# Performance work log

Hardware: AMD Instinct MI355X
Metric: run time of the kernel (lower is better)

The kernel has to match this reference:

```python
import jax, jax.numpy as jnp
import numpy as np

G, N, E, F, D = 4096, 64, 256, 64, 128
H1, H2 = 16, 2
EP = 32768
EPS = 1e-15
MAX_LOGSTD = 10.0


def setup_inputs() -> dict:
    key = jax.random.key(0)
    ks = jax.random.split(key, 16)
    def lin(k, i, o):
        return (jax.random.normal(k, (i, o), jnp.float32) / np.sqrt(i)).astype(jnp.float32)
    inp = {}
    inp["x"] = jax.random.normal(ks[0], (G, N, F), jnp.float32)
    inp["edge_index"] = jax.random.randint(ks[1], (G, 2, E), 0, N, dtype=jnp.int32)
    inp["edge_weight"] = jax.random.uniform(ks[2], (G, E), jnp.float32)
    inp["pos_edges"] = jax.random.randint(ks[3], (2, EP), 0, G, dtype=jnp.int32)
    inp["neg_edges"] = jax.random.randint(ks[4], (2, EP), 0, G, dtype=jnp.int32)
    inp["eps"] = jax.random.normal(ks[5], (G, D), jnp.float32)
    inp["W_gcn1"] = lin(ks[6], F, D); inp["b_gcn1"] = jnp.zeros((D,), jnp.float32)
    inp["W_fc1"] = lin(ks[7], D, H1); inp["b_fc1"] = jnp.zeros((H1,), jnp.float32)
    inp["W_fc2"] = lin(ks[8], H1, H2); inp["b_fc2"] = jnp.zeros((H2,), jnp.float32)
    inp["W_c1"] = lin(ks[9], D, 2 * D); inp["b_c1"] = jnp.zeros((2 * D,), jnp.float32)
    inp["W_mu"] = lin(ks[10], 2 * D, D); inp["b_mu"] = jnp.zeros((D,), jnp.float32)
    inp["W_ls"] = lin(ks[11], 2 * D, D); inp["b_ls"] = jnp.zeros((D,), jnp.float32)
    inp["emb"] = jax.random.normal(ks[12], (G, D), jnp.float32)
    inp["W_lin1"] = lin(ks[13], 2 * D, 2 * D); inp["b_lin1"] = jnp.zeros((2 * D,), jnp.float32)
    inp["W_lin2"] = lin(ks[14], 2 * D, 2 * D); inp["b_lin2"] = jnp.zeros((2 * D,), jnp.float32)
    return inp


def gcn_conv(x, src, dst, w, W, b, n):
    # PyG GCNConv: add self-loops (weight 1), sym-normalize, aggregate at target (col).
    xw = x @ W                                      # [n, out]
    deg = jnp.zeros((n,), xw.dtype).at[dst].add(w) + 1.0
    dinv = jax.lax.rsqrt(deg)
    norm = dinv[src] * w * dinv[dst]
    agg = jnp.zeros_like(xw).at[dst].add(xw[src] * norm[:, None])
    agg = agg + xw * (dinv * dinv)[:, None]         # self-loop term
    return agg + b


def sage_graph(x, ei, w, W_gcn1, b_gcn1, W_fc1, b_fc1, W_fc2, b_fc2):
    src, dst = ei[0], ei[1]
    h = gcn_conv(x, src, dst, w, W_gcn1, b_gcn1, N)          # [N, D]
    a1 = jnp.tanh(h @ W_fc1 + b_fc1)                         # [N, H1]
    S = jax.nn.softmax(a1 @ W_fc2 + b_fc2, axis=1)           # [N, 2]
    # get_laplacian(normalization='sym'): L = I - D^{-1/2} A D^{-1/2}, deg from row
    deg = jnp.zeros((N,), x.dtype).at[src].add(w)
    dinv = jnp.where(deg > 0, jax.lax.rsqrt(jnp.maximum(deg, 1e-30)), 0.0)
    lw = -dinv[src] * w * dinv[dst]
    L = jnp.zeros((N, N), x.dtype).at[src, dst].add(lw) + jnp.eye(N, dtype=x.dtype)
    new_adj = S.T @ (L @ S)                                  # [2, 2]
    norm_adj = new_adj / jnp.maximum(jnp.sum(jnp.abs(new_adj), axis=1, keepdims=True), 1e-12)
    diag = jnp.diagonal(norm_adj)
    pos_penalty = jnp.mean((diag - 1.0) ** 2)                # MSE vs ones(2)
    g_emb = jnp.mean(S.T @ h, axis=0)                        # [D]
    return g_emb, pos_penalty


def gcn_conv_unw(x, src, dst, W, b, n):
    return gcn_conv(x, src, dst, jnp.ones(src.shape, x.dtype), W, b, n)


def reference(x, edge_index, edge_weight, pos_edges, neg_edges, eps,
              W_gcn1, b_gcn1, W_fc1, b_fc1, W_fc2, b_fc2,
              W_c1, b_c1, W_mu, b_mu, W_ls, b_ls, emb,
              W_lin1, b_lin1, W_lin2, b_lin2):
    g_embs, pens = jax.vmap(sage_graph,
                            in_axes=(0, 0, 0, None, None, None, None, None, None))(
        x, edge_index, edge_weight, W_gcn1, b_gcn1, W_fc1, b_fc1, W_fc2, b_fc2)
    positive_penalty = jnp.mean(pens)
    # VGAE encode over graph-level graph (dropout in eval mode = identity)
    ps, pd = pos_edges[0], pos_edges[1]
    h = jax.nn.relu(gcn_conv_unw(g_embs, ps, pd, W_c1, b_c1, G))
    mu = gcn_conv_unw(h, ps, pd, W_mu, b_mu, G)
    logstd = jnp.minimum(gcn_conv_unw(h, ps, pd, W_ls, b_ls, G), MAX_LOGSTD)
    z = mu + eps * jnp.exp(logstd)                            # reparametrize
    zc = jnp.concatenate([emb, z], axis=-1)                   # [G, 2D]
    def pred(ei):
        fx = zc[ei[0]] @ W_lin1 + b_lin1
        fy = zc[ei[1]] @ W_lin2 + b_lin2
        return jax.nn.sigmoid(jnp.sum(fx * fy, axis=1))
    pos_pred = pred(pos_edges)
    neg_pred = pred(neg_edges)
    rec_loss = -jnp.mean(jnp.log(pos_pred + EPS)) - jnp.mean(jnp.log(1.0 - neg_pred + EPS))
    kl = -0.5 * jnp.mean(jnp.sum(1.0 + 2.0 * logstd - mu ** 2 - jnp.exp(2.0 * logstd), axis=1))
    pre_loss = rec_loss + kl / G
    return pre_loss, positive_penalty, pos_pred, neg_pred
```

## Files before the change

kernel.cpp:

```cpp
#include <hip/hip_runtime.h>
#include <hip/hip_bf16.h>
#include <math.h>

#define GG   4096
#define NNODE 64
#define EEDGE 256
#define FFEAT 64
#define DDIM 128
#define EP   32768

__device__ __forceinline__ float fast_tanh(float x) {
    float e = __expf(2.0f * x);
    return 1.0f - 2.0f / (e + 1.0f);
}

__global__ void k_prep(const float* __restrict__ Wg, const float* __restrict__ Wf1,
                       const float* __restrict__ bf1, const float* __restrict__ bg,
                       float* __restrict__ Wgf1, float* __restrict__ bcomb,
                       float* __restrict__ bg32, int* __restrict__ icnt_g) {
    int t = threadIdx.x;
    for (int o = t; o < 1024; o += 256) {
        int f = o >> 4, j = o & 15;
        float s = 0.f;
        for (int d = 0; d < 128; ++d) s += Wg[f * 128 + d] * Wf1[d * 16 + j];
        Wgf1[o] = s;
    }
    if (t < 16) {
        float s = bf1[t];
        for (int d = 0; d < 128; ++d) s += bg[d] * Wf1[d * 16 + t];
        bcomb[t] = s;
    }
    if (t >= 128) bg32[t - 128] = 32.0f * bg[t - 128];
    for (int i = t; i < 4096; i += 256) icnt_g[i] = 0;
}

__global__ __launch_bounds__(256) void k_y(
    const float* __restrict__ x, const float* __restrict__ W,
    float* __restrict__ Y)
{
    __shared__ __align__(16) float Ws[1024];
    const int t = threadIdx.x;
    *(float4*)&Ws[t * 4] = *(const float4*)&W[t * 4];
    const int rr = t >> 2, q = t & 3;
    const size_t r0 = (size_t)blockIdx.x * 256 + rr;
    const float* x0 = &x[r0 * 64];
    __syncthreads();
    float4 p0 = {0,0,0,0}, p1 = {0,0,0,0}, p2 = {0,0,0,0}, p3 = {0,0,0,0};
#pragma unroll 4
    for (int kb = 0; kb < 16; ++kb) {
        float4 xv0 = *(const float4*)&x0[kb * 4];
        float4 xv1 = *(const float4*)&x0[4096 + kb * 4];
        float4 xv2 = *(const float4*)&x0[8192 + kb * 4];
        float4 xv3 = *(const float4*)&x0[12288 + kb * 4];
#pragma unroll
        for (int kk = 0; kk < 4; ++kk) {
            float4 wv = *(const float4*)&Ws[(kb * 4 + kk) * 16 + q * 4];
            float a0 = (&xv0.x)[kk], a1 = (&xv1.x)[kk];
            float a2 = (&xv2.x)[kk], a3 = (&xv3.x)[kk];
            p0.x += a0 * wv.x; p0.y += a0 * wv.y; p0.z += a0 * wv.z; p0.w += a0 * wv.w;
            p1.x += a1 * wv.x; p1.y += a1 * wv.y; p1.z += a1 * wv.z; p1.w += a1 * wv.w;
            p2.x += a2 * wv.x; p2.y += a2 * wv.y; p2.z += a2 * wv.z; p2.w += a2 * wv.w;
            p3.x += a3 * wv.x; p3.y += a3 * wv.y; p3.z += a3 * wv.z; p3.w += a3 * wv.w;
        }
    }
    float* y0 = &Y[r0 * 16 + q * 4];
    *(float4*)&y0[0]          = p0;
    *(float4*)&y0[64 * 16]    = p1;
    *(float4*)&y0[128 * 16]   = p2;
    *(float4*)&y0[192 * 16]   = p3;
}

__global__ __launch_bounds__(256) void k_pg(
    const float* __restrict__ Yg, const int* __restrict__ ei, const float* __restrict__ ew,
    const float* __restrict__ x, const float* __restrict__ bcomb,
    const float* __restrict__ Wf2, const float* __restrict__ bf2,
    float* __restrict__ Qh, float* __restrict__ pens)
{
    __shared__ __align__(16) float sm[2624];
    float* Ys    = sm;
    int*   lsrc  = (int*)(sm + 1280);
    float* lnrm  = sm + 1536;
    int*   icnt  = (int*)(sm + 1792);
    int*   offs  = (int*)(sm + 1856);
    int*   curs  = (int*)(sm + 1920);
    float* degw  = sm + 1984;
    float* dinvs = sm + 2048;
    float* deg2s = sm + 2112;
    float* dinv2s= sm + 2176;
    float* cws   = sm + 2240;
    float* Ss    = sm + 2304;
    float* LSs   = sm + 2432;
    float* bcs   = sm + 2560;
    float* Wf2s  = sm + 2576;
    float* bf2s  = sm + 2608;

    const int g = blockIdx.x;
    const int t = threadIdx.x;
    const int n = t >> 2, q = t & 3;

    int es, ed; float wv;
    {
        const int* eg = ei + (size_t)g * 512;
        es = eg[t];
        ed = eg[256 + t];
        wv = ew[(size_t)g * 256 + t];
        *(float4*)&Ys[n * 20 + q * 4] = *(const float4*)&Yg[(size_t)g * 1024 + t * 4];
        if (t < 16) bcs[t] = bcomb[t];
        if (t < 32) Wf2s[t] = Wf2[t];
        if (t < 2)  bf2s[t] = bf2[t];
        if (t < 64) { icnt[t] = 0; degw[t] = 1.0f; deg2s[t] = 0.0f; }
        if (t < 128) LSs[t] = 0.0f;
    }
    __syncthreads();

    atomicAdd(&icnt[ed], 1);
    atomicAdd(&degw[ed], wv);
    atomicAdd(&deg2s[es], wv);
    __syncthreads();

    if (t < 64) {
        int v = icnt[t], own = v;
        for (int o = 1; o < 64; o <<= 1) { int u = __shfl_up(v, o); if (t >= o) v += u; }
        int excl = v - own;
        offs[t] = excl; curs[t] = excl;
        float dv = rsqrtf(degw[t]);
        dinvs[t] = dv;
        cws[t] = dv * dv;
        float dg = deg2s[t];
        dinv2s[t] = dg > 0.0f ? rsqrtf(fmaxf(dg, 1e-30f)) : 0.0f;
    }
    __syncthreads();

    float lw;
    {
        int pos = atomicAdd(&curs[ed], 1);
        float nm = dinvs[es] * wv * dinvs[ed];
        lsrc[pos] = es;
        lnrm[pos] = nm;
        atomicAdd(&cws[es], nm);
        lw = -dinv2s[es] * wv * dinv2s[ed];
    }
    __syncthreads();

    {
        float dv = dinvs[n];
        float sc = dv * dv;
        float4 acc = *(const float4*)&Ys[n * 20 + q * 4];
        acc.x *= sc; acc.y *= sc; acc.z *= sc; acc.w *= sc;
        int o = offs[n], c = icnt[n];
        for (int j = 0; j < c; ++j) {
            int s = lsrc[o + j];
            float nm = lnrm[o + j];
            float4 yv = *(const float4*)&Ys[s * 20 + q * 4];
            acc.x += yv.x * nm; acc.y += yv.y * nm;
            acc.z += yv.z * nm; acc.w += yv.w * nm;
        }
        float4 bc4 = *(const float4*)&bcs[q * 4];
        float t0 = fast_tanh(acc.x + bc4.x);
        float t1 = fast_tanh(acc.y + bc4.y);
        float t2 = fast_tanh(acc.z + bc4.z);
        float t3 = fast_tanh(acc.w + bc4.w);
        float4 wf0 = *(const float4*)&Wf2s[8 * q];
        float4 wf1 = *(const float4*)&Wf2s[8 * q + 4];
        float z0 = t0 * wf0.x + t1 * wf0.z + t2 * wf1.x + t3 * wf1.z;
        float z1 = t0 * wf0.y + t1 * wf0.w + t2 * wf1.y + t3 * wf1.w;
        z0 += __shfl_xor(z0, 1); z0 += __shfl_xor(z0, 2);
        z1 += __shfl_xor(z1, 1); z1 += __shfl_xor(z1, 2);
        if (q == 0) {
            z0 += bf2s[0]; z1 += bf2s[1];
            float m = fmaxf(z0, z1);
            float e0 = __expf(z0 - m), e1 = __expf(z1 - m);
            float inv = 1.0f / (e0 + e1);
            Ss[n * 2] = e0 * inv; Ss[n * 2 + 1] = e1 * inv;
        }
    }
    __syncthreads();

    {
        float s0 = Ss[ed * 2], s1 = Ss[ed * 2 + 1];
        atomicAdd(&LSs[es * 2],     lw * s0);
        atomicAdd(&LSs[es * 2 + 1], lw * s1);
    }
    __syncthreads();

    if (t < 64) {
        float s0 = Ss[t * 2], s1 = Ss[t * 2 + 1];
        float l0 = s0 + LSs[t * 2], l1 = s1 + LSs[t * 2 + 1];
        float p00 = s0 * l0, p01 = s0 * l1, p10 = s1 * l0, p11 = s1 * l1;
        for (int o = 32; o; o >>= 1) {
            p00 += __shfl_down(p00, o); p01 += __shfl_down(p01, o);
            p10 += __shfl_down(p10, o); p11 += __shfl_down(p11, o);
        }
        if (t == 0) {
            float r0 = fmaxf(fabsf(p00) + fabsf(p01), 1e-12f);
            float r1 = fmaxf(fabsf(p10) + fabsf(p11), 1e-12f);
            float d0 = p00 / r0 - 1.0f, d1 = p11 / r1 - 1.0f;
            pens[g] = 0.5f * (d0 * d0 + d1 * d1);
        }
    }
    {
        int k = t & 63, p = t >> 6;
        const float* xg = x + (size_t)g * 4096 + k;
        float qk = 0.f;
#pragma unroll 4
        for (int nn = p * 16; nn < p * 16 + 16; ++nn)
            qk += cws[nn] * xg[(size_t)nn * 64];
        __syncthreads();
        Ys[p * 64 + k] = qk;
    }
    __syncthreads();
    if (t < 64)
        Qh[(size_t)g * 64 + t] = 0.5f * (Ys[t] + Ys[64 + t] + Ys[128 + t] + Ys[192 + t]);
}

__global__ void k_cnt(const int* __restrict__ pd, int* __restrict__ icnt) {
    int e = blockIdx.x * 256 + threadIdx.x;
    atomicAdd(&icnt[pd[e]], 1);
}

__global__ void k_scan(const int* __restrict__ icnt, int* __restrict__ offs,
                       int* __restrict__ curs, float* __restrict__ dinv) {
    __shared__ int wsum[4];
    int t = threadIdx.x;
    int base = t * 16;
    int l0,l1,l2,l3,l4,l5,l6,l7,l8,l9,l10,l11,l12,l13,l14,l15;
    l0=icnt[base+0]; l1=icnt[base+1]; l2=icnt[base+2]; l3=icnt[base+3];
    l4=icnt[base+4]; l5=icnt[base+5]; l6=icnt[base+6]; l7=icnt[base+7];
    l8=icnt[base+8]; l9=icnt[base+9]; l10=icnt[base+10]; l11=icnt[base+11];
    l12=icnt[base+12]; l13=icnt[base+13]; l14=icnt[base+14]; l15=icnt[base+15];
    int s = l0+l1+l2+l3+l4+l5+l6+l7+l8+l9+l10+l11+l12+l13+l14+l15;
    int lane = t & 63, w = t >> 6;
    int v = s;
    for (int o = 1; o < 64; o <<= 1) { int u = __shfl_up(v, o); if (lane >= o) v += u; }
    if (lane == 63) wsum[w] = v;
    __syncthreads();
    int woff = 0;
    for (int i = 0; i < 4; ++i) if (i < w) woff += wsum[i];
    int run = woff + v - s;
#define SC(L, I) offs[base+(I)] = run; curs[base+(I)] = run; \
    dinv[base+(I)] = rsqrtf((float)(L) + 1.0f); run += L;
    SC(l0,0) SC(l1,1) SC(l2,2) SC(l3,3) SC(l4,4) SC(l5,5) SC(l6,6) SC(l7,7)
    SC(l8,8) SC(l9,9) SC(l10,10) SC(l11,11) SC(l12,12) SC(l13,13) SC(l14,14) SC(l15,15)
#undef SC
}

__global__ void k_place(const int* __restrict__ pe, const float* __restrict__ dinv,
                        int* __restrict__ curs, int* __restrict__ csr_src,
                        float* __restrict__ csr_nrm) {
    int e = blockIdx.x * 256 + threadIdx.x;
    int s = pe[e], d = pe[EP + e];
    int pos = atomicAdd(&curs[d], 1);
    csr_src[pos] = s;
    csr_nrm[pos] = dinv[s] * dinv[d];
}

__global__ void k_gather128(const int* __restrict__ offs, const int* __restrict__ icnt,
                            const int* __restrict__ csr_src, const float* __restrict__ csr_nrm,
                            const float* __restrict__ dinv, const float* __restrict__ in,
                            float* __restrict__ out) {
    int g = blockIdx.x, d = threadIdx.x;
    float dv = dinv[g];
    float acc = in[(size_t)g * 128 + d] * dv * dv;
    int o = offs[g], c = icnt[g];
    for (int j = 0; j < c; ++j)
        acc += in[(size_t)csr_src[o + j] * 128 + d] * csr_nrm[o + j];
    out[(size_t)g * 128 + d] = acc;
}

__global__ void k_gather256(const int* __restrict__ offs, const int* __restrict__ icnt,
                            const int* __restrict__ csr_src, const float* __restrict__ csr_nrm,
                            const float* __restrict__ dinv, const float* __restrict__ in,
                            float* __restrict__ out) {
    int g = blockIdx.x, d = threadIdx.x;
    float dv = dinv[g];
    float acc = in[(size_t)g * 256 + d] * dv * dv;
    int o = offs[g], c = icnt[g];
    for (int j = 0; j < c; ++j)
        acc += in[(size_t)csr_src[o + j] * 256 + d] * csr_nrm[o + j];
    out[(size_t)g * 256 + d] = acc;
}

__global__ __launch_bounds__(256) void k_gemm(
    const float* __restrict__ A,
    const float* __restrict__ B0, const float* __restrict__ bias0, float* __restrict__ C0,
    const float* __restrict__ B1, const float* __restrict__ bias1, float* __restrict__ C1,
    int M, int K, int N, int dorelu)
{
    __shared__ __align__(16) float lds[2 * 4352];
    const float* B = B0; const float* bias = bias0; float* C = C0;
    int by = blockIdx.y;
    if (B1 != nullptr && by >= (int)(gridDim.y >> 1)) {
        B = B1; bias = bias1; C = C1; by -= (gridDim.y >> 1);
    }
    const int mb = blockIdx.x * 64, nbb = by * 64;
    const int t = threadIdx.x;
    const int tm4 = (t >> 4) * 4, tn4 = (t & 15) * 4;
    const int ma = t >> 2, ka = (t & 3) * 8;
    const int kb = t >> 3, nb8 = (t & 7) * 8;

    float4 pa0, pa1, pb0, pb1;
#define LOADT(K0) { \
    const float* Ap = &A[(size_t)(mb + ma) * K + (K0) + ka]; \
    pa0 = *(const float4*)Ap; pa1 = *(const float4*)(Ap + 4); \
    const float* Bp = &B[(size_t)((K0) + kb) * N + nbb + nb8]; \
    pb0 = *(const float4*)Bp; pb1 = *(const float4*)(Bp + 4); }
#define STORET(BUF) { \
    float* At_ = lds + (BUF) * 4352; \
    At_[(ka + 0) * 68 + ma] = pa0.x; At_[(ka + 1) * 68 + ma] = pa0.y; \
    At_[(ka + 2) * 68 + ma] = pa0.z; At_[(ka + 3) * 68 + ma] = pa0.w; \
    At_[(ka + 4) * 68 + ma] = pa1.x; At_[(ka + 5) * 68 + ma] = pa1.y; \
    At_[(ka + 6) * 68 + ma] = pa1.z; At_[(ka + 7) * 68 + ma] = pa1.w; \
    float* Bs_ = lds + (BUF) * 4352 + 2176; \
    *(float4*)&Bs_[kb * 68 + nb8] = pb0; *(float4*)&Bs_[kb * 68 + nb8 + 4] = pb1; }

    float4 ca0 = {0,0,0,0}, ca1 = {0,0,0,0}, ca2 = {0,0,0,0}, ca3 = {0,0,0,0};
    const int nk0 = K >> 5;
    LOADT(0)
    STORET(0)
    __syncthreads();
    for (int it = 0; it < nk0; ++it) {
        if (it + 1 < nk0) LOADT((it + 1) * 32)
        const float* At_ = lds + (it & 1) * 4352;
        const float* Bs_ = At_ + 2176;
#pragma unroll
        for (int k = 0; k < 32; ++k) {
            float4 av = *(const float4*)&At_[k * 68 + tm4];
            float4 bv = *(const float4*)&Bs_[k * 68 + tn4];
            ca0.x += av.x * bv.x; ca0.y += av.x * bv.y; ca0.z += av.x * bv.z; ca0.w += av.x * bv.w;
            ca1.x += av.y * bv.x; ca1.y += av.y * bv.y; ca1.z += av.y * bv.z; ca1.w += av.y * bv.w;
            ca2.x += av.z * bv.x; ca2.y += av.z * bv.y; ca2.z += av.z * bv.z; ca2.w += av.z * bv.w;
            ca3.x += av.w * bv.x; ca3.y += av.w * bv.y; ca3.z += av.w * bv.z; ca3.w += av.w * bv.w;
        }
        if (it + 1 < nk0) {
            STORET((it + 1) & 1)
            __syncthreads();
        }
    }
#undef LOADT
#undef STORET
    float4 bv4 = {0, 0, 0, 0};
    if (bias) bv4 = *(const float4*)&bias[nbb + tn4];
#define CST(I, CV) { \
    float4 v; v.x = CV.x + bv4.x; v.y = CV.y + bv4.y; v.z = CV.z + bv4.z; v.w = CV.w + bv4.w; \
    if (dorelu) { v.x = fmaxf(v.x, 0.f); v.y = fmaxf(v.y, 0.f); v.z = fmaxf(v.z, 0.f); v.w = fmaxf(v.w, 0.f); } \
    *(float4*)&C[(size_t)(mb + tm4 + (I)) * N + nbb + tn4] = v; }
    CST(0, ca0) CST(1, ca1) CST(2, ca2) CST(3, ca3)
#undef CST
}

__global__ void k_fin_z(const float* __restrict__ mu_arr, const float* __restrict__ ls_arr,
                        const float* __restrict__ eps, const float* __restrict__ emb,
                        float* __restrict__ zc, float* __restrict__ klp) {
    __shared__ float smw[2];
    int g = blockIdx.x, d = threadIdx.x;
    int idx = g * 128 + d;
    float mu = mu_arr[idx];
    float ls = fminf(ls_arr[idx], 10.0f);
    float e  = __expf(ls);
    float z = mu + eps[idx] * e;
    zc[(size_t)g * 256 + d] = emb[idx];
    zc[(size_t)g * 256 + 128 + d] = z;
    float term = 1.0f + 2.0f * ls - mu * mu - e * e;
    for (int o = 32; o; o >>= 1) term += __shfl_down(term, o);
    if ((d & 63) == 0) smw[d >> 6] = term;
    __syncthreads();
    if (d == 0) klp[g] = smw[0] + smw[1];
}

__global__ void k_pred(const float* __restrict__ A, const float* __restrict__ B,
                       const int* __restrict__ pos, const int* __restrict__ neg,
                       float* __restrict__ out, float* __restrict__ predp) {
    __shared__ float smw[16];
    int t = threadIdx.x, sub = t >> 4, l = t & 15;
    int eg = blockIdx.x * 16 + sub;
    int isneg = eg >= EP;
    int e = eg - (isneg ? EP : 0);
    const int* eix = isneg ? neg : pos;
    int s = eix[e], d = eix[EP + e];
    const float4* Ar = (const float4*)(A + (size_t)s * 256);
    const float4* Br = (const float4*)(B + (size_t)d * 256);
    float dot = 0.f;
#pragma unroll
    for (int q = 0; q < 4; ++q) {
        float4 av = Ar[l + 16 * q], bv = Br[l + 16 * q];
        dot += av.x * bv.x + av.y * bv.y + av.z * bv.z + av.w * bv.w;
    }
    for (int o = 8; o; o >>= 1) dot += __shfl_down(dot, o);
    if (l == 0) {
        float p = 1.0f / (1.0f + __expf(-dot));
        float term;
        if (isneg) { out[2 + EP + e] = p; term = __logf(1.0f - p + 1e-15f); }
        else       { out[2 + e] = p;      term = __logf(p + 1e-15f); }
        smw[sub] = term;
    }
    __syncthreads();
    if (t == 0) {
        float s16 = 0.f;
#pragma unroll
        for (int i = 0; i < 16; ++i) s16 += smw[i];
        predp[blockIdx.x] = s16;
    }
}

__global__ void k_final(const float* __restrict__ pens, const float* __restrict__ klp,
                        const float* __restrict__ predp, float* __restrict__ out) {
    __shared__ float sm[16];
    int t = threadIdx.x;
    float s_pen = 0.f, s_kl = 0.f, s_pos = 0.f, s_neg = 0.f;
    for (int i = t; i < 4096; i += 256) { s_pen += pens[i]; s_kl += klp[i]; }
    for (int i = t; i < 2048; i += 256) { s_pos += predp[i]; s_neg += predp[2048 + i]; }
    for (int o = 32; o; o >>= 1) {
        s_pen += __shfl_down(s_pen, o); s_kl += __shfl_down(s_kl, o);
        s_pos += __shfl_down(s_pos, o); s_neg += __shfl_down(s_neg, o);
    }
    int w = t >> 6;
    if ((t & 63) == 0) { sm[w] = s_pen; sm[4 + w] = s_kl; sm[8 + w] = s_pos; sm[12 + w] = s_neg; }
    __syncthreads();
    if (t == 0) {
        float pen = sm[0] + sm[1] + sm[2] + sm[3];
        float kls = sm[4] + sm[5] + sm[6] + sm[7];
        float pos = sm[8] + sm[9] + sm[10] + sm[11];
        float neg = sm[12] + sm[13] + sm[14] + sm[15];
        float rec = -(pos / 32768.0f) - (neg / 32768.0f);
        out[0] = rec - 0.5f * kls / (4096.0f * 4096.0f);
        out[1] = pen * (1.0f / 4096.0f);
    }
}

extern "C" void kernel_launch(void* const* d_in, const int* in_sizes, int n_in,
                              void* d_out, int out_size, void* d_ws, size_t ws_size,
                              hipStream_t stream) {
    const float* x   = (const float*)d_in[0];
    const int*   ei  = (const int*)d_in[1];
    const float* ew  = (const float*)d_in[2];
    const int*   pos = (const int*)d_in[3];
    const int*   neg = (const int*)d_in[4];
    const float* eps = (const float*)d_in[5];
    const float* Wg  = (const float*)d_in[6];
    const float* bg  = (const float*)d_in[7];
    const float* Wf1 = (const float*)d_in[8];
    const float* bf1 = (const float*)d_in[9];
    const float* Wf2 = (const float*)d_in[10];
    const float* bf2 = (const float*)d_in[11];
    const float* Wc1 = (const float*)d_in[12];
    const float* bc1 = (const float*)d_in[13];
    const float* Wmu = (const float*)d_in[14];
    const float* bmu = (const float*)d_in[15];
    const float* Wls = (const float*)d_in[16];
    const float* bls = (const float*)d_in[17];
    const float* emb = (const float*)d_in[18];
    const float* Wl1 = (const float*)d_in[19];
    const float* bl1 = (const float*)d_in[20];
    const float* Wl2 = (const float*)d_in[21];
    const float* bl2 = (const float*)d_in[22];
    float* out = (float*)d_out;
    float* ws  = (float*)d_ws;

    float* g_embs  = ws + 0;
    float* dinv    = ws + 524288;
    int*   icnt_g  = (int*)(ws + 528384);
    int*   off_g   = (int*)(ws + 532480);
    int*   cur_g   = (int*)(ws + 536576);
    int*   csr_src = (int*)(ws + 540672);
    float* csr_nrm = ws + 573440;
    float* Qh      = ws + 606208;
    float* ga      = ws + 868352;
    float* h       = ws + 1392640;
    float* ha      = ws + 2441216;
    float* mu_arr  = ws + 3489792;
    float* ls_arr  = ws + 4014080;
    float* zc      = ws + 4538368;
    float* Abuf    = ws + 5586944;
    float* Bbuf    = ws + 6635520;
    float* pens    = ws + 7684096;
    float* klp     = ws + 7688192;
    float* predp   = ws + 7692288;
    float* Wgf1    = ws + 7708672;
    float* bcomb   = ws + 7709696;
    float* bg32    = ws + 7709712;
    float* Y       = ws + 1392640;

    k_prep<<<1, 256, 0, stream>>>(Wg, Wf1, bf1, bg, Wgf1, bcomb, bg32, icnt_g);
    k_y<<<1024, 256, 0, stream>>>(x, Wgf1, Y);
    k_pg<<<GG, 256, 0, stream>>>(Y, ei, ew, x, bcomb, Wf2, bf2, Qh, pens);
    k_gemm<<<dim3(64, 2), 256, 0, stream>>>(Qh, Wg, bg32, g_embs,
                                            nullptr, nullptr, nullptr, GG, 64, 128, 0);

    k_cnt<<<EP / 256, 256, 0, stream>>>(pos + EP, icnt_g);
    k_scan<<<1, 256, 0, stream>>>(icnt_g, off_g, cur_g, dinv);
    k_place<<<EP / 256, 256, 0, stream>>>(pos, dinv, cur_g, csr_src, csr_nrm);

    k_gather128<<<GG, 128, 0, stream>>>(off_g, icnt_g, csr_src, csr_nrm, dinv, g_embs, ga);
    k_gemm<<<dim3(64, 4), 256, 0, stream>>>(ga, Wc1, bc1, h,
                                            nullptr, nullptr, nullptr, GG, 128, 256, 1);

    k_gather256<<<GG, 256, 0, stream>>>(off_g, icnt_g, csr_src, csr_nrm, dinv, h, ha);
    k_gemm<<<dim3(64, 4), 256, 0, stream>>>(ha, Wmu, bmu, mu_arr,
                                            Wls, bls, ls_arr, GG, 256, 128, 0);
    k_fin_z<<<GG, 128, 0, stream>>>(mu_arr, ls_arr, eps, emb, zc, klp);

    k_gemm<<<dim3(64, 8), 256, 0, stream>>>(zc, Wl1, bl1, Abuf,
                                            Wl2, bl2, Bbuf, GG, 256, 256, 0);

    k_pred<<<(2 * EP) / 16, 256, 0, stream>>>(Abuf, Bbuf, pos, neg, out, predp);
    k_final<<<1, 256, 0, stream>>>(pens, klp, predp, out);
}
```

Measured before the change: 337.9 us.

## Fuse Qh@Wg projection into k_pg, prefetch x rows, restructure k_y

```diff
diff --git a/kernel.cpp b/kernel.cpp
--- a/kernel.cpp
+++ b/kernel.cpp
@@ -38,43 +38,44 @@
     const float* __restrict__ x, const float* __restrict__ W,
     float* __restrict__ Y)
 {
-    __shared__ __align__(16) float Ws[1024];
     const int t = threadIdx.x;
-    *(float4*)&Ws[t * 4] = *(const float4*)&W[t * 4];
-    const int rr = t >> 2, q = t & 3;
-    const size_t r0 = (size_t)blockIdx.x * 256 + rr;
-    const float* x0 = &x[r0 * 64];
-    __syncthreads();
-    float4 p0 = {0,0,0,0}, p1 = {0,0,0,0}, p2 = {0,0,0,0}, p3 = {0,0,0,0};
-#pragma unroll 4
-    for (int kb = 0; kb < 16; ++kb) {
-        float4 xv0 = *(const float4*)&x0[kb * 4];
-        float4 xv1 = *(const float4*)&x0[4096 + kb * 4];
-        float4 xv2 = *(const float4*)&x0[8192 + kb * 4];
-        float4 xv3 = *(const float4*)&x0[12288 + kb * 4];
-#pragma unroll
-        for (int kk = 0; kk < 4; ++kk) {
-            float4 wv = *(const float4*)&Ws[(kb * 4 + kk) * 16 + q * 4];
-            float a0 = (&xv0.x)[kk], a1 = (&xv1.x)[kk];
-            float a2 = (&xv2.x)[kk], a3 = (&xv3.x)[kk];
-            p0.x += a0 * wv.x; p0.y += a0 * wv.y; p0.z += a0 * wv.z; p0.w += a0 * wv.w;
-            p1.x += a1 * wv.x; p1.y += a1 * wv.y; p1.z += a1 * wv.z; p1.w += a1 * wv.w;
-            p2.x += a2 * wv.x; p2.y += a2 * wv.y; p2.z += a2 * wv.z; p2.w += a2 * wv.w;
-            p3.x += a3 * wv.x; p3.y += a3 * wv.y; p3.z += a3 * wv.z; p3.w += a3 * wv.w;
-        }
-    }
-    float* y0 = &Y[r0 * 16 + q * 4];
-    *(float4*)&y0[0]          = p0;
-    *(float4*)&y0[64 * 16]    = p1;
-    *(float4*)&y0[128 * 16]   = p2;
-    *(float4*)&y0[192 * 16]   = p3;
+    const int rr = t >> 4, jq = (t >> 2) & 3, q = t & 3;
+    float4 w[16];
+#pragma unroll
+    for (int kk = 0; kk < 16; ++kk)
+        w[kk] = *(const float4*)&W[(q * 16 + kk) * 16 + jq * 4];
+    const size_t rbase = (size_t)blockIdx.x * 256;
+#pragma unroll 2
+    for (int it = 0; it < 16; ++it) {
+        const int n = it * 16 + rr;
+        const float* xr = &x[(rbase + n) * 64 + q * 16];
+        float xv[16];
+        *(float4*)&xv[0]  = *(const float4*)&xr[0];
+        *(float4*)&xv[4]  = *(const float4*)&xr[4];
+        *(float4*)&xv[8]  = *(const float4*)&xr[8];
+        *(float4*)&xv[12] = *(const float4*)&xr[12];
+        float4 acc = {0.f, 0.f, 0.f, 0.f};
+#pragma unroll
+        for (int kk = 0; kk < 16; ++kk) {
+            float a = xv[kk];
+            acc.x += a * w[kk].x; acc.y += a * w[kk].y;
+            acc.z += a * w[kk].z; acc.w += a * w[kk].w;
+        }
+        acc.x += __shfl_xor(acc.x, 1); acc.x += __shfl_xor(acc.x, 2);
+        acc.y += __shfl_xor(acc.y, 1); acc.y += __shfl_xor(acc.y, 2);
+        acc.z += __shfl_xor(acc.z, 1); acc.z += __shfl_xor(acc.z, 2);
+        acc.w += __shfl_xor(acc.w, 1); acc.w += __shfl_xor(acc.w, 2);
+        if (q == 0)
+            *(float4*)&Y[(rbase + n) * 16 + jq * 4] = acc;
+    }
 }
 
 __global__ __launch_bounds__(256) void k_pg(
     const float* __restrict__ Yg, const int* __restrict__ ei, const float* __restrict__ ew,
     const float* __restrict__ x, const float* __restrict__ bcomb,
     const float* __restrict__ Wf2, const float* __restrict__ bf2,
-    float* __restrict__ Qh, float* __restrict__ pens)
+    const float* __restrict__ Wg, const float* __restrict__ bg32,
+    float* __restrict__ g_embs, float* __restrict__ pens)
 {
     __shared__ __align__(16) float sm[2624];
     float* Ys    = sm;
@@ -97,14 +98,20 @@
     const int g = blockIdx.x;
     const int t = threadIdx.x;
     const int n = t >> 2, q = t & 3;
+    const int k9 = t & 63, p9 = t >> 6;
 
     int es, ed; float wv;
+    float xreg[16];
     {
         const int* eg = ei + (size_t)g * 512;
         es = eg[t];
         ed = eg[256 + t];
         wv = ew[(size_t)g * 256 + t];
         *(float4*)&Ys[n * 20 + q * 4] = *(const float4*)&Yg[(size_t)g * 1024 + t * 4];
+        const float* xg = x + (size_t)g * 4096 + k9;
+#pragma unroll
+        for (int i = 0; i < 16; ++i)
+            xreg[i] = xg[(size_t)(p9 * 16 + i) * 64];
         if (t < 16) bcs[t] = bcomb[t];
         if (t < 32) Wf2s[t] = Wf2[t];
         if (t < 2)  bf2s[t] = bf2[t];
@@ -199,18 +206,29 @@
         }
     }
     {
-        int k = t & 63, p = t >> 6;
-        const float* xg = x + (size_t)g * 4096 + k;
         float qk = 0.f;
-#pragma unroll 4
-        for (int nn = p * 16; nn < p * 16 + 16; ++nn)
-            qk += cws[nn] * xg[(size_t)nn * 64];
-        __syncthreads();
-        Ys[p * 64 + k] = qk;
-    }
-    __syncthreads();
+#pragma unroll
+        for (int i = 0; i < 16; ++i)
+            qk += cws[p9 * 16 + i] * xreg[i];
+        Ys[p9 * 64 + k9] = qk;
+    }
+    __syncthreads();
+    float* qhs = lnrm;
     if (t < 64)
-        Qh[(size_t)g * 64 + t] = 0.5f * (Ys[t] + Ys[64 + t] + Ys[128 + t] + Ys[192 + t]);
+        qhs[t] = 0.5f * (Ys[t] + Ys[64 + t] + Ys[128 + t] + Ys[192 + t]);
+    __syncthreads();
+
+    {
+        const int d = t >> 1, half = t & 1;
+        const float* Wc = Wg + (size_t)half * 32 * 128 + d;
+        float acc = 0.f;
+#pragma unroll
+        for (int kk = 0; kk < 32; ++kk)
+            acc += qhs[half * 32 + kk] * Wc[(size_t)kk * 128];
+        acc += __shfl_xor(acc, 1);
+        if (half == 0)
+            g_embs[(size_t)g * 128 + d] = acc + bg32[d];
+    }
 }
 
 __global__ void k_cnt(const int* __restrict__ pd, int* __restrict__ icnt) {
@@ -463,7 +481,6 @@
     int*   cur_g   = (int*)(ws + 536576);
     int*   csr_src = (int*)(ws + 540672);
     float* csr_nrm = ws + 573440;
-    float* Qh      = ws + 606208;
     float* ga      = ws + 868352;
     float* h       = ws + 1392640;
     float* ha      = ws + 2441216;
@@ -482,9 +499,8 @@
 
     k_prep<<<1, 256, 0, stream>>>(Wg, Wf1, bf1, bg, Wgf1, bcomb, bg32, icnt_g);
     k_y<<<1024, 256, 0, stream>>>(x, Wgf1, Y);
-    k_pg<<<GG, 256, 0, stream>>>(Y, ei, ew, x, bcomb, Wf2, bf2, Qh, pens);
-    k_gemm<<<dim3(64, 2), 256, 0, stream>>>(Qh, Wg, bg32, g_embs,
-                                            nullptr, nullptr, nullptr, GG, 64, 128, 0);
+    k_pg<<<GG, 256, 0, stream>>>(Y, ei, ew, x, bcomb, Wf2, bf2, Wg, bg32,
+                                 g_embs, pens);
 
     k_cnt<<<EP / 256, 256, 0, stream>>>(pos + EP, icnt_g);
     k_scan<<<1, 256, 0, stream>>>(icnt_g, off_g, cur_g, dinv);
```

Measured after the change: 339.3 us. No clear change (+0.4%).
